# Performance work log

Measured on AMD Instinct MI355X. Metric: run time of the kernel, lower is better.

## Reference

```python
import jax, jax.numpy as jnp
import numpy as np

N_NODES = 512      # nodes in the original graph
N_SUB = 512        # NodeDeleted -> one subgraph per node
E_SUB = 2097152    # edges in the union-of-subgraphs graph (avg degree 8)
E_ORIG = 8192      # edges in the original graph
IN_DIM = 64
EMB = 64
L = 4
TASKS = 10


def setup_inputs() -> dict:
    key = jax.random.key(0)
    ks = jax.random.split(key, 16)
    NT = N_NODES * N_SUB
    x = jax.random.normal(ks[0], (NT, IN_DIM), jnp.float32)
    # edges stay within a subgraph: global id = subgraph_id * N + local id
    eg = jax.random.randint(ks[1], (E_SUB,), 0, N_SUB)
    src = jax.random.randint(ks[2], (E_SUB,), 0, N_NODES)
    dst = jax.random.randint(ks[3], (E_SUB,), 0, N_NODES)
    edge_index = jnp.stack([eg * N_NODES + src, eg * N_NODES + dst]).astype(jnp.int32)
    original_edge_index = jax.random.randint(ks[4], (2, E_ORIG), 0, N_NODES).astype(jnp.int32)
    subgraph_node_idx = jnp.tile(jnp.arange(N_NODES, dtype=jnp.int32), N_SUB)
    subgraph_batch = jnp.repeat(jnp.arange(N_SUB, dtype=jnp.int32), N_NODES)
    p = lambda k, shape: jax.random.normal(k, shape, jnp.float32) * 0.05
    return dict(
        x=x,
        Wrel=p(ks[5], (L, EMB, IN_DIM)), brel=jnp.zeros((L, EMB), jnp.float32),
        Wroot=p(ks[6], (L, EMB, IN_DIM)),
        bn_gamma=jnp.ones((L, EMB), jnp.float32), bn_beta=jnp.zeros((L, EMB), jnp.float32),
        Wrel_s=p(ks[7], (L, EMB, IN_DIM)), brel_s=jnp.zeros((L, EMB), jnp.float32),
        Wroot_s=p(ks[8], (L, EMB, IN_DIM)),
        bns_gamma=jnp.ones((L, EMB), jnp.float32), bns_beta=jnp.zeros((L, EMB), jnp.float32),
        W1=p(ks[9], (2 * EMB, EMB)), b1=jnp.zeros((2 * EMB,), jnp.float32),
        W2=p(ks[10], (TASKS, 2 * EMB)), b2=jnp.zeros((TASKS,), jnp.float32),
        edge_index=edge_index, original_edge_index=original_edge_index,
        subgraph_node_idx=subgraph_node_idx, subgraph_batch=subgraph_batch,
        num_nodes_int=N_NODES,
    )


def _gconv(h, ei, Wr, br, Wt, n):
    # PyG GraphConv, aggr='add': lin_rel(sum_{j->i} x_j) + lin_root(x_i)
    agg = jax.ops.segment_sum(h[ei[0]], ei[1], num_segments=n)
    return agg @ Wr.T + br + h @ Wt.T


def _bn(h, g, b):
    # BatchNorm1d, training mode: biased batch stats, eps=1e-5
    mu = h.mean(0)
    var = ((h - mu) ** 2).mean(0)
    return (h - mu) * jax.lax.rsqrt(var + 1e-5) * g + b


def _smean(src, idx, n):
    s = jax.ops.segment_sum(src, idx, num_segments=n)
    c = jax.ops.segment_sum(jnp.ones((src.shape[0], 1), src.dtype), idx, num_segments=n)
    return s / jnp.maximum(c, 1.0)


def reference(x, Wrel, brel, Wroot, bn_gamma, bn_beta, Wrel_s, brel_s, Wroot_s,
              bns_gamma, bns_beta, W1, b1, W2, b2,
              edge_index, original_edge_index, subgraph_node_idx, subgraph_batch,
              num_nodes_int):
    N = num_nodes_int
    NT = x.shape[0]
    S = NT // N  # num_subgraphs
    h = x
    for i in range(Wrel.shape[0]):
        h1 = _bn(_gconv(h, edge_index, Wrel[i], brel[i], Wroot[i], NT),
                 bn_gamma[i], bn_beta[i])
        x_sum = _smean(h, subgraph_node_idx, N)              # [N, emb]
        h2 = _bn(_gconv(x_sum, original_edge_index, Wrel_s[i], brel_s[i], Wroot_s[i], N),
                 bns_gamma[i], bns_beta[i])
        h = jax.nn.relu(h1 + jnp.tile(h2, (S, 1)))           # broadcast h2 to every subgraph
    x_nodes = _smean(h, subgraph_node_idx, N)                # [N, emb]
    z = jax.nn.log_softmax(x_nodes, axis=-1)                 # log_softmax BEFORE final MLP (as in source)
    out = jax.nn.relu(z @ W1.T + b1) @ W2.T + b2             # [N, num_tasks]
    return out
```

## Files before the change

### kernel.cpp

```cpp
#include <hip/hip_runtime.h>
#include <math.h>

#define NT 262144
#define NS 512
#define ES 2097152
#define EO 8192
#define NLAYER 4
#define WROW 68
#define BSL 704
#define EREG 8192

typedef short bf16x8 __attribute__((ext_vector_type(8)));
typedef float f32x4 __attribute__((ext_vector_type(4)));

__device__ __forceinline__ void cvt_hilo(const float* v, bf16x8* hi, bf16x8* lo) {
    union U { bf16x8 v; unsigned u[4]; };
    U H, L;
    #pragma unroll
    for (int q = 0; q < 4; q++) {
        float v0 = v[2 * q], v1 = v[2 * q + 1];
        unsigned h01;
        asm("v_cvt_pk_bf16_f32 %0, %1, %2" : "=v"(h01) : "v"(v0), "v"(v1));
        float l0 = v0 - __uint_as_float(h01 << 16);
        float l1 = v1 - __uint_as_float(h01 & 0xffff0000u);
        unsigned l01;
        asm("v_cvt_pk_bf16_f32 %0, %1, %2" : "=v"(l01) : "v"(l0), "v"(l1));
        H.u[q] = h01; L.u[q] = l01;
    }
    *hi = H.v; *lo = L.v;
}

__global__ __launch_bounds__(256) void bucket_kernel(const int* __restrict__ ei,
        int* __restrict__ gcur, unsigned* __restrict__ rbuf) {
    __shared__ int lcnt[512];
    __shared__ int lcur[512];
    int p = blockIdx.x;
    int g = p & 7;
    int base = p * 4096;
    int tid = threadIdx.x;
    for (int t = tid; t < 512; t += 256) lcnt[t] = 0;
    __syncthreads();
    int subs[16];
    unsigned recs[16];
    #pragma unroll
    for (int j = 0; j < 16; j++) {
        int e = base + j * 256 + tid;
        int d = ei[ES + e];
        int srcl = ei[e] & 511;
        subs[j] = d >> 9;
        recs[j] = (unsigned)srcl | ((unsigned)(d & 511) << 16);
        atomicAdd(&lcnt[subs[j]], 1);
    }
    __syncthreads();
    for (int t = tid; t < 512; t += 256) {
        int c = lcnt[t];
        lcur[t] = c ? atomicAdd(&gcur[g * 512 + t], c) : 0;
    }
    __syncthreads();
    #pragma unroll
    for (int j = 0; j < 16; j++) {
        int s = subs[j];
        int pos = atomicAdd(&lcur[s], 1);
        if (pos < BSL) rbuf[((size_t)s * 8 + g) * BSL + pos] = recs[j];
    }
}

__global__ __launch_bounds__(512) void csr_sub_kernel(const int* __restrict__ gcur,
        const unsigned* __restrict__ rbuf, int* __restrict__ rowptr,
        unsigned short* __restrict__ ebuf) {
    __shared__ int sdeg[512];
    __shared__ int sscan[512];
    __shared__ int scur[512];
    __shared__ unsigned short erow[EREG];
    __shared__ int scnt[8];
    int s = blockIdx.x;
    int t = threadIdx.x;
    sdeg[t] = 0;
    if (t < 8) scnt[t] = min(gcur[t * 512 + s], BSL);
    unsigned* e32 = (unsigned*)erow;
    #pragma unroll
    for (int j = 0; j < 8; j++) e32[j * 512 + t] = 0x02000200u;
    __syncthreads();
    for (int g = 0; g < 8; g++) {
        int cg = scnt[g];
        const unsigned* rb = rbuf + ((size_t)s * 8 + g) * BSL;
        for (int i = t; i < cg; i += 512) atomicAdd(&sdeg[rb[i] >> 16], 1);
    }
    __syncthreads();
    int pdeg = (sdeg[t] + 3) & ~3;
    sscan[t] = pdeg;
    __syncthreads();
    for (int off = 1; off < 512; off <<= 1) {
        int x = (t >= off) ? sscan[t - off] : 0;
        __syncthreads();
        sscan[t] += x;
        __syncthreads();
    }
    int excl = sscan[t] - pdeg;
    scur[t] = excl;
    rowptr[s * 513 + t] = s * EREG + excl;
    if (t == 511) rowptr[s * 513 + 512] = s * EREG + sscan[511];
    __syncthreads();
    for (int g = 0; g < 8; g++) {
        int cg = scnt[g];
        const unsigned* rb = rbuf + ((size_t)s * 8 + g) * BSL;
        for (int i = t; i < cg; i += 512) {
            unsigned rec = rb[i];
            int pos = atomicAdd(&scur[rec >> 16], 1);
            erow[pos] = (unsigned short)(rec & 511);
        }
    }
    __syncthreads();
    uint4* eo = (uint4*)(ebuf + (size_t)s * EREG);
    const uint4* ei4 = (const uint4*)erow;
    eo[t] = ei4[t];
    eo[t + 512] = ei4[t + 512];
}

__global__ void small_csr_kernel(const int* __restrict__ oei, int* __restrict__ rowptrS,
                                 int* __restrict__ srcsS) {
    __shared__ int sdeg[NS];
    __shared__ int scur[NS];
    int t = threadIdx.x;
    if (t < NS) sdeg[t] = 0;
    __syncthreads();
    for (int e = t; e < EO; e += 1024) atomicAdd(&sdeg[oei[EO + e]], 1);
    __syncthreads();
    int myv = (t < NS) ? sdeg[t] : 0;
    __syncthreads();
    for (int off = 1; off < NS; off <<= 1) {
        int x = (t >= off && t < NS) ? sdeg[t - off] : 0;
        __syncthreads();
        if (t < NS) sdeg[t] += x;
        __syncthreads();
    }
    if (t < NS) {
        int excl = sdeg[t] - myv;
        rowptrS[t] = excl;
        scur[t] = excl;
        if (t == 0) rowptrS[NS] = EO;
    }
    __syncthreads();
    for (int e = t; e < EO; e += 1024) {
        int d = oei[EO + e];
        int pos = atomicAdd(&scur[d], 1);
        srcsS[pos] = oei[e];
    }
}

__global__ __launch_bounds__(512, 2) void gconv_sub_kernel(
    const float* __restrict__ hsrc,
    const float* __restrict__ h2,
    const float* __restrict__ stB, const float* __restrict__ stS,
    const float* __restrict__ gB, const float* __restrict__ bB,
    const float* __restrict__ gS, const float* __restrict__ bS,
    int mode,
    const int* __restrict__ rowptr, const unsigned short* __restrict__ ebuf,
    const float* __restrict__ Wr, const float* __restrict__ Wt,
    const float* __restrict__ br,
    float* __restrict__ hout, float* __restrict__ stats)
{
    extern __shared__ char smem[];
    float* Wn = (float*)smem;
    float* bnp = Wn + 513 * WROW;

    int p = blockIdx.x;
    int sub = p;
    int tid = threadIdx.x;
    int w = tid >> 6;
    int l = tid & 63;
    int cl = l & 15;
    int kg = l >> 4;
    int kg8 = kg * 8;
    int half = w >> 2;
    int m = w & 3;

    if (mode) {
        if (tid < 64) {
            int c = tid;
            float sb = 0.f, qb = 0.f, ss = 0.f, qs = 0.f;
            for (int r2 = 0; r2 < 32; r2++) {
                sb += stB[r2 * 128 + c];
                qb += stB[r2 * 128 + 64 + c];
                ss += stS[r2 * 128 + c];
                qs += stS[r2 * 128 + 64 + c];
            }
            float muB = sb * (1.f / 262144.f);
            float varB = qb * (1.f / 262144.f) - muB * muB;
            float scB = gB[c] * rsqrtf(varB + 1e-5f);
            bnp[c] = scB;
            bnp[64 + c] = bB[c] - muB * scB;
            float muS = ss * (1.f / 512.f);
            float varS = qs * (1.f / 512.f) - muS * muS;
            float scS = gS[c] * rsqrtf(varS + 1e-5f);
            bnp[128 + c] = scS;
            bnp[192 + c] = bS[c] - muS * scS;
        }
        __syncthreads();
    }

    const float* srcbase = hsrc + (size_t)sub * 512 * 64;
    for (int idx = tid; idx < 512 * 16; idx += 512) {
        int r = idx >> 4;
        int c4 = (idx & 15) * 4;
        float4 a = *(const float4*)(srcbase + r * 64 + c4);
        if (mode) {
            float4 b = *(const float4*)(h2 + r * 64 + c4);
            float4 sB4 = *(const float4*)(bnp + c4);
            float4 hB4 = *(const float4*)(bnp + 64 + c4);
            float4 sS4 = *(const float4*)(bnp + 128 + c4);
            float4 hS4 = *(const float4*)(bnp + 192 + c4);
            a.x = fmaxf(a.x * sB4.x + hB4.x + b.x * sS4.x + hS4.x, 0.f);
            a.y = fmaxf(a.y * sB4.y + hB4.y + b.y * sS4.y + hS4.y, 0.f);
            a.z = fmaxf(a.z * sB4.z + hB4.z + b.z * sS4.z + hS4.z, 0.f);
            a.w = fmaxf(a.w * sB4.w + hB4.w + b.w * sS4.w + hS4.w, 0.f);
        }
        *(float4*)(Wn + r * WROW + c4) = a;
    }
    if (tid < WROW) Wn[512 * WROW + tid] = 0.f;

    bf16x8 Bh[16], Bl[16];
    float bias0, bias1, bias2, bias3;
    #pragma unroll
    for (int c = 0; c < 4; c++) {
        int col = c * 16 + cl;
        #pragma unroll
        for (int ch = 0; ch < 4; ch++) {
            const float* mat = (ch < 2) ? Wr : Wt;
            int k = (ch & 1) * 32 + kg8;
            float vv[8];
            *(float4*)vv = *(const float4*)(mat + col * 64 + k);
            *(float4*)(vv + 4) = *(const float4*)(mat + col * 64 + k + 4);
            cvt_hilo(vv, &Bh[c * 4 + ch], &Bl[c * 4 + ch]);
        }
    }
    bias0 = br[cl];
    bias1 = br[16 + cl];
    bias2 = br[32 + cl];
    bias3 = br[48 + cl];

    const uint2* ebuf2 = (const uint2*)ebuf;
    __syncthreads();

#define GATH1(qv) { \
        const float* pp = Wn + (qv) * WROW + kg8; \
        float4 tg0 = *(const float4*)(pp); \
        float4 tg1 = *(const float4*)(pp + 4); \
        float4 tg2 = *(const float4*)(pp + 32); \
        float4 tg3 = *(const float4*)(pp + 36); \
        a0.x += tg0.x; a0.y += tg0.y; a0.z += tg0.z; a0.w += tg0.w; \
        a1.x += tg1.x; a1.y += tg1.y; a1.z += tg1.z; a1.w += tg1.w; \
        a2.x += tg2.x; a2.y += tg2.y; a2.z += tg2.z; a2.w += tg2.w; \
        a3.x += tg3.x; a3.y += tg3.y; a3.z += tg3.z; a3.w += tg3.w; \
    }

#define DO_CHUNK(g0h, g1h, ch) { \
        float gg[8]; \
        *(float4*)gg = g0h; *(float4*)(gg + 4) = g1h; \
        bf16x8 ah, al; \
        cvt_hilo(gg, &ah, &al); \
        acc0 = __builtin_amdgcn_mfma_f32_16x16x32_bf16(ah, Bh[0 * 4 + ch], acc0, 0, 0, 0); \
        acc1 = __builtin_amdgcn_mfma_f32_16x16x32_bf16(ah, Bh[1 * 4 + ch], acc1, 0, 0, 0); \
        acc2 = __builtin_amdgcn_mfma_f32_16x16x32_bf16(ah, Bh[2 * 4 + ch], acc2, 0, 0, 0); \
        acc3 = __builtin_amdgcn_mfma_f32_16x16x32_bf16(ah, Bh[3 * 4 + ch], acc3, 0, 0, 0); \
        acc0 = __builtin_amdgcn_mfma_f32_16x16x32_bf16(al, Bh[0 * 4 + ch], acc0, 0, 0, 0); \
        acc1 = __builtin_amdgcn_mfma_f32_16x16x32_bf16(al, Bh[1 * 4 + ch], acc1, 0, 0, 0); \
        acc2 = __builtin_amdgcn_mfma_f32_16x16x32_bf16(al, Bh[2 * 4 + ch], acc2, 0, 0, 0); \
        acc3 = __builtin_amdgcn_mfma_f32_16x16x32_bf16(al, Bh[3 * 4 + ch], acc3, 0, 0, 0); \
        acc0 = __builtin_amdgcn_mfma_f32_16x16x32_bf16(ah, Bl[0 * 4 + ch], acc0, 0, 0, 0); \
        acc1 = __builtin_amdgcn_mfma_f32_16x16x32_bf16(ah, Bl[1 * 4 + ch], acc1, 0, 0, 0); \
        acc2 = __builtin_amdgcn_mfma_f32_16x16x32_bf16(ah, Bl[2 * 4 + ch], acc2, 0, 0, 0); \
        acc3 = __builtin_amdgcn_mfma_f32_16x16x32_bf16(ah, Bl[3 * 4 + ch], acc3, 0, 0, 0); \
    }

    float s0 = 0.f, s1 = 0.f, s2 = 0.f, s3 = 0.f;
    float q0s = 0.f, q1s = 0.f, q2s = 0.f, q3s = 0.f;

    for (int tt = 0; tt < 4; tt++) {
        int tile = half * 4 + tt;
        int nb = sub * 512 + tile * 64;
        int row = tile * 64 + m * 16 + cl;
        int rpb = sub * 513;
        int e0q = rowptr[rpb + row] >> 2;
        int e1q = rowptr[rpb + row + 1] >> 2;

        float4 a0 = make_float4(0.f, 0.f, 0.f, 0.f);
        float4 a1 = a0, a2 = a0, a3 = a0;
        uint2 rr = make_uint2(0u, 0u);
        int u = e0q;
        if (u < e1q) rr = ebuf2[u];
        while (u < e1q) {
            uint2 cur = rr;
            ++u;
            if (u < e1q) rr = ebuf2[u];
            unsigned q0 = cur.x & 0xffffu;
            unsigned q1 = cur.x >> 16;
            unsigned q2 = cur.y & 0xffffu;
            unsigned q3 = cur.y >> 16;
            GATH1(q0);
            GATH1(q1);
            GATH1(q2);
            GATH1(q3);
        }

        const float* wrow = Wn + (size_t)(tile * 64 + m * 16 + cl) * WROW + kg8;
        float4 r0 = *(const float4*)(wrow);
        float4 r1 = *(const float4*)(wrow + 4);
        float4 r2 = *(const float4*)(wrow + 32);
        float4 r3 = *(const float4*)(wrow + 36);

        f32x4 acc0, acc1, acc2, acc3;
        #pragma unroll
        for (int j = 0; j < 4; j++) {
            acc0[j] = bias0; acc1[j] = bias1; acc2[j] = bias2; acc3[j] = bias3;
        }
        DO_CHUNK(a0, a1, 0);
        DO_CHUNK(a2, a3, 1);
        DO_CHUNK(r0, r1, 2);
        DO_CHUNK(r2, r3, 3);

        int node0 = nb + m * 16 + kg * 4;
        #pragma unroll
        for (int j = 0; j < 4; j++) {
            float v0 = acc0[j], v1 = acc1[j], v2 = acc2[j], v3 = acc3[j];
            size_t rowb = (size_t)(node0 + j) * 64;
            hout[rowb + cl] = v0;
            hout[rowb + 16 + cl] = v1;
            hout[rowb + 32 + cl] = v2;
            hout[rowb + 48 + cl] = v3;
            s0 += v0; q0s += v0 * v0;
            s1 += v1; q1s += v1 * v1;
            s2 += v2; q2s += v2 * v2;
            s3 += v3; q3s += v3 * v3;
        }
    }

    s0 += __shfl_xor(s0, 16, 64); s0 += __shfl_xor(s0, 32, 64);
    s1 += __shfl_xor(s1, 16, 64); s1 += __shfl_xor(s1, 32, 64);
    s2 += __shfl_xor(s2, 16, 64); s2 += __shfl_xor(s2, 32, 64);
    s3 += __shfl_xor(s3, 16, 64); s3 += __shfl_xor(s3, 32, 64);
    q0s += __shfl_xor(q0s, 16, 64); q0s += __shfl_xor(q0s, 32, 64);
    q1s += __shfl_xor(q1s, 16, 64); q1s += __shfl_xor(q1s, 32, 64);
    q2s += __shfl_xor(q2s, 16, 64); q2s += __shfl_xor(q2s, 32, 64);
    q3s += __shfl_xor(q3s, 16, 64); q3s += __shfl_xor(q3s, 32, 64);
    if (kg == 0) {
        int rep = p & 31;
        atomicAdd(&stats[rep * 128 + cl], s0);
        atomicAdd(&stats[rep * 128 + 16 + cl], s1);
        atomicAdd(&stats[rep * 128 + 32 + cl], s2);
        atomicAdd(&stats[rep * 128 + 48 + cl], s3);
        atomicAdd(&stats[rep * 128 + 64 + cl], q0s);
        atomicAdd(&stats[rep * 128 + 80 + cl], q1s);
        atomicAdd(&stats[rep * 128 + 96 + cl], q2s);
        atomicAdd(&stats[rep * 128 + 112 + cl], q3s);
    }
#undef GATH1
#undef DO_CHUNK
}

__global__ __launch_bounds__(512, 6) void gconv_kernel(
    const float* __restrict__ hin, const int* __restrict__ rowptr, const int* __restrict__ srcs,
    const float* __restrict__ Wr, const float* __restrict__ Wt, const float* __restrict__ br,
    float* __restrict__ hout, float* __restrict__ stats)
{
    __shared__ float wrt[4096];
    __shared__ float wtt[4096];
    __shared__ float4 aggT[8][64];
    __shared__ float4 hT[8][64];
    __shared__ float sbuf[8][64];
    __shared__ float qbuf[8][64];
    __shared__ float brs[64];

    int tid = threadIdx.x;
    for (int idx = tid; idx < 4096; idx += 512) {
        int cc = idx >> 6, kk = idx & 63;
        wrt[kk * 64 + ((kk + cc) & 63)] = Wr[idx];
        wtt[kk * 64 + ((kk + cc) & 63)] = Wt[idx];
    }
    if (tid < 64) brs[tid] = br[tid];
    __syncthreads();

    int w = tid >> 6;
    int c = tid & 63;
    int node0 = (blockIdx.x * 8 + w) * 4;

    float* aggp = (float*)&aggT[w][0];
    float* hp   = (float*)&hT[w][0];
    #pragma unroll
    for (int r = 0; r < 4; r++) {
        int node = node0 + r;
        hp[c * 4 + r] = hin[node * 64 + c];
        int e0 = rowptr[node], e1 = rowptr[node + 1];
        float a = 0.f;
        int e = e0;
        for (; e + 4 <= e1; e += 4) {
            int s0 = srcs[e], s1 = srcs[e + 1], s2 = srcs[e + 2], s3 = srcs[e + 3];
            float v0 = hin[s0 * 64 + c];
            float v1 = hin[s1 * 64 + c];
            float v2 = hin[s2 * 64 + c];
            float v3 = hin[s3 * 64 + c];
            a += (v0 + v1) + (v2 + v3);
        }
        for (; e < e1; e++) a += hin[srcs[e] * 64 + c];
        aggp[c * 4 + r] = a;
    }

    float o0 = brs[c], o1 = o0, o2 = o0, o3 = o0;
    #pragma unroll 8
    for (int k = 0; k < 64; k++) {
        float wr = wrt[k * 64 + ((k + c) & 63)];
        float wt = wtt[k * 64 + ((k + c) & 63)];
        float4 av = aggT[w][k];
        float4 hv = hT[w][k];
        o0 += wr * av.x + wt * hv.x;
        o1 += wr * av.y + wt * hv.y;
        o2 += wr * av.z + wt * hv.z;
        o3 += wr * av.w + wt * hv.w;
    }
    hout[(node0 + 0) * 64 + c] = o0;
    hout[(node0 + 1) * 64 + c] = o1;
    hout[(node0 + 2) * 64 + c] = o2;
    hout[(node0 + 3) * 64 + c] = o3;

    sbuf[w][c] = (o0 + o1) + (o2 + o3);
    qbuf[w][c] = (o0 * o0 + o1 * o1) + (o2 * o2 + o3 * o3);
    __syncthreads();
    int rep = blockIdx.x & 31;
    if (w == 0) {
        float s = 0.f;
        #pragma unroll
        for (int ww = 0; ww < 8; ww++) s += sbuf[ww][c];
        atomicAdd(&stats[rep * 128 + c], s);
    } else if (w == 1) {
        float q = 0.f;
        #pragma unroll
        for (int ww = 0; ww < 8; ww++) q += qbuf[ww][c];
        atomicAdd(&stats[rep * 128 + 64 + c], q);
    }
}

__global__ __launch_bounds__(1024) void xsum_kernel(
    const float* __restrict__ hsrc, const float* __restrict__ h2,
    const float* __restrict__ stB, const float* __restrict__ stS,
    const float* __restrict__ gB, const float* __restrict__ bB,
    const float* __restrict__ gS, const float* __restrict__ bS,
    int mode, float* __restrict__ xsum)
{
    __shared__ float bnp[256];
    __shared__ float red[16][64];
    int t = threadIdx.x;
    if (mode) {
        if (t < 64) {
            int c = t;
            float sb = 0.f, qb = 0.f, ss = 0.f, qs = 0.f;
            for (int r2 = 0; r2 < 32; r2++) {
                sb += stB[r2 * 128 + c];
                qb += stB[r2 * 128 + 64 + c];
                ss += stS[r2 * 128 + c];
                qs += stS[r2 * 128 + 64 + c];
            }
            float muB = sb * (1.f / 262144.f);
            float varB = qb * (1.f / 262144.f) - muB * muB;
            float scB = gB[c] * rsqrtf(varB + 1e-5f);
            bnp[c] = scB;
            bnp[64 + c] = bB[c] - muB * scB;
            float muS = ss * (1.f / 512.f);
            float varS = qs * (1.f / 512.f) - muS * muS;
            float scS = gS[c] * rsqrtf(varS + 1e-5f);
            bnp[128 + c] = scS;
            bnp[192 + c] = bS[c] - muS * scS;
        }
        __syncthreads();
    }

    int w = t >> 6;
    int l = t & 63;
    int c4 = (l & 15) * 4;
    int r = l >> 4;
    int n = blockIdx.x;

    float bx = 0.f, by = 0.f, bz = 0.f, bw = 0.f;
    float4 sB = make_float4(1.f, 1.f, 1.f, 1.f);
    float4 hB = make_float4(0.f, 0.f, 0.f, 0.f);
    if (mode) {
        sB = *(const float4*)(bnp + c4);
        hB = *(const float4*)(bnp + 64 + c4);
        float4 sS = *(const float4*)(bnp + 128 + c4);
        float4 hS = *(const float4*)(bnp + 192 + c4);
        float4 b2 = *(const float4*)(h2 + n * 64 + c4);
        bx = b2.x * sS.x + hS.x;
        by = b2.y * sS.y + hS.y;
        bz = b2.z * sS.z + hS.z;
        bw = b2.w * sS.w + hS.w;
    }

    float4 acc = make_float4(0.f, 0.f, 0.f, 0.f);
    #pragma unroll
    for (int j = 0; j < 8; j++) {
        int si = w * 32 + j * 4 + r;
        size_t base = (size_t)(si * 512 + n) * 64 + c4;
        float4 a = *(const float4*)(hsrc + base);
        float4 v;
        if (mode) {
            v.x = fmaxf(a.x * sB.x + hB.x + bx, 0.f);
            v.y = fmaxf(a.y * sB.y + hB.y + by, 0.f);
            v.z = fmaxf(a.z * sB.z + hB.z + bz, 0.f);
            v.w = fmaxf(a.w * sB.w + hB.w + bw, 0.f);
        } else {
            v = a;
        }
        acc.x += v.x; acc.y += v.y; acc.z += v.z; acc.w += v.w;
    }
    acc.x += __shfl_xor(acc.x, 16, 64); acc.y += __shfl_xor(acc.y, 16, 64);
    acc.z += __shfl_xor(acc.z, 16, 64); acc.w += __shfl_xor(acc.w, 16, 64);
    acc.x += __shfl_xor(acc.x, 32, 64); acc.y += __shfl_xor(acc.y, 32, 64);
    acc.z += __shfl_xor(acc.z, 32, 64); acc.w += __shfl_xor(acc.w, 32, 64);
    if (l < 16) {
        red[w][c4 + 0] = acc.x;
        red[w][c4 + 1] = acc.y;
        red[w][c4 + 2] = acc.z;
        red[w][c4 + 3] = acc.w;
    }
    __syncthreads();
    if (t < 64) {
        float tot = 0.f;
        #pragma unroll
        for (int ww = 0; ww < 16; ww++) tot += red[ww][t];
        xsum[n * 64 + t] = tot * (1.f / 512.f);
    }
}

__global__ void head_kernel(const float* __restrict__ xs, const float* __restrict__ W1,
                            const float* __restrict__ b1, const float* __restrict__ W2,
                            const float* __restrict__ b2, float* __restrict__ out) {
    __shared__ float z[64];
    __shared__ float hid[128];
    int t = threadIdx.x;
    int n = blockIdx.x;
    if (t < 64) {
        float v = xs[n * 64 + t];
        float m = v;
        for (int off = 32; off >= 1; off >>= 1) m = fmaxf(m, __shfl_xor(m, off, 64));
        float e = expf(v - m);
        float s = e;
        for (int off = 32; off >= 1; off >>= 1) s += __shfl_xor(s, off, 64);
        z[t] = v - m - logf(s);
    }
    __syncthreads();
    {
        float acc = b1[t];
        const float* wrow = W1 + t * 64;
        #pragma unroll 8
        for (int k = 0; k < 64; k++) acc += z[k] * wrow[k];
        hid[t] = fmaxf(acc, 0.f);
    }
    __syncthreads();
    if (t < 10) {
        float o = b2[t];
        const float* wrow = W2 + t * 128;
        #pragma unroll 8
        for (int j = 0; j < 128; j++) o += hid[j] * wrow[j];
        out[n * 10 + t] = o;
    }
}

extern "C" void kernel_launch(void* const* d_in, const int* in_sizes, int n_in,
                              void* d_out, int out_size, void* d_ws, size_t ws_size,
                              hipStream_t stream) {
    const float* x       = (const float*)d_in[0];
    const float* Wrel    = (const float*)d_in[1];
    const float* brel    = (const float*)d_in[2];
    const float* Wroot   = (const float*)d_in[3];
    const float* bn_g    = (const float*)d_in[4];
    const float* bn_b    = (const float*)d_in[5];
    const float* Wrel_s  = (const float*)d_in[6];
    const float* brel_s  = (const float*)d_in[7];
    const float* Wroot_s = (const float*)d_in[8];
    const float* bns_g   = (const float*)d_in[9];
    const float* bns_b   = (const float*)d_in[10];
    const float* W1      = (const float*)d_in[11];
    const float* b1      = (const float*)d_in[12];
    const float* W2      = (const float*)d_in[13];
    const float* b2      = (const float*)d_in[14];
    const int* ei        = (const int*)d_in[15];
    const int* oei       = (const int*)d_in[16];
    float* out = (float*)d_out;

    char* ws = (char*)d_ws;
    size_t off = 0;
    auto alloc = [&](size_t bytes) -> void* {
        void* p = ws + off;
        off = (off + bytes + 255) & ~(size_t)255;
        return p;
    };
    float* h1    = (float*)alloc((size_t)NT * 64 * 4);
    float* xsum  = (float*)alloc(NS * 64 * 4);
    float* h2    = (float*)alloc(NS * 64 * 4);
    float* stats = (float*)alloc(NLAYER * 2 * 4096 * 4);
    int* rowptr  = (int*)alloc((size_t)NS * 513 * 4);
    int* gcur    = (int*)alloc(8 * 512 * 4);
    unsigned short* ebuf = (unsigned short*)alloc((size_t)NS * EREG * 2);
    int* rowptrS = (int*)alloc(513 * 4);
    int* srcsS   = (int*)alloc(EO * 4);
    unsigned* rbuf = (unsigned*)h1;
    (void)ws_size; (void)in_sizes; (void)n_in; (void)out_size;

    hipMemsetAsync(gcur, 0, 8 * 512 * 4, stream);
    hipMemsetAsync(stats, 0, (size_t)NLAYER * 2 * 4096 * 4, stream);

    bucket_kernel<<<ES / 4096, 256, 0, stream>>>(ei, gcur, rbuf);
    csr_sub_kernel<<<NS, 512, 0, stream>>>(gcur, rbuf, rowptr, ebuf);
    small_csr_kernel<<<1, 1024, 0, stream>>>(oei, rowptrS, srcsS);

    const size_t SMEM = (513 * WROW + 256) * 4;

    for (int i = 0; i < NLAYER; i++) {
        int mode = (i > 0);
        const float* hsrc = mode ? h1 : x;
        const float* stPB = stats + (i - 1) * 8192;
        const float* stPS = stPB + 4096;
        const float* gBp = bn_g + (i - 1) * 64;
        const float* bBp = bn_b + (i - 1) * 64;
        const float* gSp = bns_g + (i - 1) * 64;
        const float* bSp = bns_b + (i - 1) * 64;
        float* stB = stats + i * 8192;
        float* stS = stB + 4096;

        xsum_kernel<<<NS, 1024, 0, stream>>>(hsrc, h2, stPB, stPS, gBp, bBp, gSp, bSp,
                                             mode, xsum);
        gconv_sub_kernel<<<NS, 512, SMEM, stream>>>(hsrc, h2, stPB, stPS,
            gBp, bBp, gSp, bSp, mode, rowptr, ebuf,
            Wrel + i * 4096, Wroot + i * 4096, brel + i * 64, h1, stB);
        gconv_kernel<<<NS / 32, 512, 0, stream>>>(xsum, rowptrS, srcsS,
            Wrel_s + i * 4096, Wroot_s + i * 4096, brel_s + i * 64, h2, stS);
    }
    {
        const float* stPB = stats + 3 * 8192;
        const float* stPS = stPB + 4096;
        xsum_kernel<<<NS, 1024, 0, stream>>>(h1, h2, stPB, stPS,
            bn_g + 3 * 64, bn_b + 3 * 64, bns_g + 3 * 64, bns_b + 3 * 64, 1, xsum);
    }
    head_kernel<<<NS, 128, 0, stream>>>(xsum, W1, b1, W2, b2, out);
}
```

Baseline: 568.7 us.

## Fuse small-graph GraphConv into subgraph kernel and store node features as fp16 in LDS

New measurement: 716.5 us. +26.0%, slower.

```diff
diff --git a/kernel.cpp b/kernel.cpp
--- a/kernel.cpp
+++ b/kernel.cpp
@@ -6,12 +6,14 @@
 #define ES 2097152
 #define EO 8192
 #define NLAYER 4
-#define WROW 68
+#define WROWH 72
 #define BSL 704
 #define EREG 8192
 
 typedef short bf16x8 __attribute__((ext_vector_type(8)));
 typedef float f32x4 __attribute__((ext_vector_type(4)));
+typedef _Float16 half8 __attribute__((ext_vector_type(8)));
+typedef _Float16 half4v __attribute__((ext_vector_type(4)));
 
 __device__ __forceinline__ void cvt_hilo(const float* v, bf16x8* hi, bf16x8* lo) {
     union U { bf16x8 v; unsigned u[4]; };
@@ -148,7 +150,7 @@
     }
 }
 
-__global__ __launch_bounds__(512, 2) void gconv_sub_kernel(
+__global__ __launch_bounds__(512, 4) void gconv_sub_kernel(
     const float* __restrict__ hsrc,
     const float* __restrict__ h2,
     const float* __restrict__ stB, const float* __restrict__ stS,
@@ -158,15 +160,98 @@
     const int* __restrict__ rowptr, const unsigned short* __restrict__ ebuf,
     const float* __restrict__ Wr, const float* __restrict__ Wt,
     const float* __restrict__ br,
-    float* __restrict__ hout, float* __restrict__ stats)
+    float* __restrict__ hout, float* __restrict__ stats,
+    const float* __restrict__ xsumIn, const int* __restrict__ rowptrS,
+    const int* __restrict__ srcsS, const float* __restrict__ WrS,
+    const float* __restrict__ WtS, const float* __restrict__ brS,
+    float* __restrict__ h2out, float* __restrict__ statsS)
 {
     extern __shared__ char smem[];
-    float* Wn = (float*)smem;
-    float* bnp = Wn + 513 * WROW;
+    int tid = threadIdx.x;
+
+    if (blockIdx.x >= NS) {
+        float* wrt = (float*)smem;
+        float* wtt = wrt + 4096;
+        float4* aggT = (float4*)(wtt + 4096);
+        float4* hT = aggT + 8 * 64;
+        float* sbuf = (float*)(hT + 8 * 64);
+        float* qbuf = sbuf + 512;
+        float* brs = qbuf + 512;
+        int b2 = blockIdx.x - NS;
+
+        for (int idx = tid; idx < 4096; idx += 512) {
+            int cc = idx >> 6, kk = idx & 63;
+            wrt[kk * 64 + ((kk + cc) & 63)] = WrS[idx];
+            wtt[kk * 64 + ((kk + cc) & 63)] = WtS[idx];
+        }
+        if (tid < 64) brs[tid] = brS[tid];
+        __syncthreads();
+
+        int w = tid >> 6;
+        int c = tid & 63;
+        int node0 = (b2 * 8 + w) * 4;
+
+        float* aggp = (float*)&aggT[w * 64];
+        float* hp   = (float*)&hT[w * 64];
+        #pragma unroll
+        for (int r = 0; r < 4; r++) {
+            int node = node0 + r;
+            hp[c * 4 + r] = xsumIn[node * 64 + c];
+            int e0 = rowptrS[node], e1 = rowptrS[node + 1];
+            float a = 0.f;
+            int e = e0;
+            for (; e + 4 <= e1; e += 4) {
+                int s0 = srcsS[e], s1 = srcsS[e + 1], s2 = srcsS[e + 2], s3 = srcsS[e + 3];
+                float v0 = xsumIn[s0 * 64 + c];
+                float v1 = xsumIn[s1 * 64 + c];
+                float v2 = xsumIn[s2 * 64 + c];
+                float v3 = xsumIn[s3 * 64 + c];
+                a += (v0 + v1) + (v2 + v3);
+            }
+            for (; e < e1; e++) a += xsumIn[srcsS[e] * 64 + c];
+            aggp[c * 4 + r] = a;
+        }
+
+        float o0 = brs[c], o1 = o0, o2 = o0, o3 = o0;
+        #pragma unroll 8
+        for (int k = 0; k < 64; k++) {
+            float wr = wrt[k * 64 + ((k + c) & 63)];
+            float wt = wtt[k * 64 + ((k + c) & 63)];
+            float4 av = aggT[w * 64 + k];
+            float4 hv = hT[w * 64 + k];
+            o0 += wr * av.x + wt * hv.x;
+            o1 += wr * av.y + wt * hv.y;
+            o2 += wr * av.z + wt * hv.z;
+            o3 += wr * av.w + wt * hv.w;
+        }
+        h2out[(node0 + 0) * 64 + c] = o0;
+        h2out[(node0 + 1) * 64 + c] = o1;
+        h2out[(node0 + 2) * 64 + c] = o2;
+        h2out[(node0 + 3) * 64 + c] = o3;
+
+        sbuf[w * 64 + c] = (o0 + o1) + (o2 + o3);
+        qbuf[w * 64 + c] = (o0 * o0 + o1 * o1) + (o2 * o2 + o3 * o3);
+        __syncthreads();
+        int rep = b2 & 31;
+        if (w == 0) {
+            float s = 0.f;
+            #pragma unroll
+            for (int ww = 0; ww < 8; ww++) s += sbuf[ww * 64 + c];
+            atomicAdd(&statsS[rep * 128 + c], s);
+        } else if (w == 1) {
+            float q = 0.f;
+            #pragma unroll
+            for (int ww = 0; ww < 8; ww++) q += qbuf[ww * 64 + c];
+            atomicAdd(&statsS[rep * 128 + 64 + c], q);
+        }
+        return;
+    }
+
+    _Float16* WnH = (_Float16*)smem;
+    float* bnp = (float*)(smem + 513 * WROWH * 2);
 
     int p = blockIdx.x;
     int sub = p;
-    int tid = threadIdx.x;
     int w = tid >> 6;
     int l = tid & 63;
     int cl = l & 15;
@@ -215,9 +300,12 @@
             a.z = fmaxf(a.z * sB4.z + hB4.z + b.z * sS4.z + hS4.z, 0.f);
             a.w = fmaxf(a.w * sB4.w + hB4.w + b.w * sS4.w + hS4.w, 0.f);
         }
-        *(float4*)(Wn + r * WROW + c4) = a;
-    }
-    if (tid < WROW) Wn[512 * WROW + tid] = 0.f;
+        half4v hv;
+        hv[0] = (_Float16)a.x; hv[1] = (_Float16)a.y;
+        hv[2] = (_Float16)a.z; hv[3] = (_Float16)a.w;
+        *(half4v*)(WnH + r * WROWH + c4) = hv;
+    }
+    if (tid < 32) ((unsigned*)(WnH + 512 * WROWH))[tid] = 0u;
 
     bf16x8 Bh[16], Bl[16];
     float bias0, bias1, bias2, bias3;
@@ -243,15 +331,13 @@
     __syncthreads();
 
 #define GATH1(qv) { \
-        const float* pp = Wn + (qv) * WROW + kg8; \
-        float4 tg0 = *(const float4*)(pp); \
-        float4 tg1 = *(const float4*)(pp + 4); \
-        float4 tg2 = *(const float4*)(pp + 32); \
-        float4 tg3 = *(const float4*)(pp + 36); \
-        a0.x += tg0.x; a0.y += tg0.y; a0.z += tg0.z; a0.w += tg0.w; \
-        a1.x += tg1.x; a1.y += tg1.y; a1.z += tg1.z; a1.w += tg1.w; \
-        a2.x += tg2.x; a2.y += tg2.y; a2.z += tg2.z; a2.w += tg2.w; \
-        a3.x += tg3.x; a3.y += tg3.y; a3.z += tg3.z; a3.w += tg3.w; \
+        const _Float16* pp = WnH + (unsigned)(qv) * WROWH + kg8; \
+        half8 h0 = *(const half8*)(pp); \
+        half8 h1v = *(const half8*)(pp + 32); \
+        a0.x += (float)h0[0]; a0.y += (float)h0[1]; a0.z += (float)h0[2]; a0.w += (float)h0[3]; \
+        a1.x += (float)h0[4]; a1.y += (float)h0[5]; a1.z += (float)h0[6]; a1.w += (float)h0[7]; \
+        a2.x += (float)h1v[0]; a2.y += (float)h1v[1]; a2.z += (float)h1v[2]; a2.w += (float)h1v[3]; \
+        a3.x += (float)h1v[4]; a3.y += (float)h1v[5]; a3.z += (float)h1v[6]; a3.w += (float)h1v[7]; \
     }
 
 #define DO_CHUNK(g0h, g1h, ch) { \
@@ -303,11 +389,13 @@
             GATH1(q3);
         }
 
-        const float* wrow = Wn + (size_t)(tile * 64 + m * 16 + cl) * WROW + kg8;
-        float4 r0 = *(const float4*)(wrow);
-        float4 r1 = *(const float4*)(wrow + 4);
-        float4 r2 = *(const float4*)(wrow + 32);
-        float4 r3 = *(const float4*)(wrow + 36);
+        const _Float16* wrowH = WnH + (unsigned)(tile * 64 + m * 16 + cl) * WROWH + kg8;
+        half8 rh0 = *(const half8*)(wrowH);
+        half8 rh1 = *(const half8*)(wrowH + 32);
+        float4 r0 = make_float4((float)rh0[0], (float)rh0[1], (float)rh0[2], (float)rh0[3]);
+        float4 r1 = make_float4((float)rh0[4], (float)rh0[5], (float)rh0[6], (float)rh0[7]);
+        float4 r2 = make_float4((float)rh1[0], (float)rh1[1], (float)rh1[2], (float)rh1[3]);
+        float4 r3 = make_float4((float)rh1[4], (float)rh1[5], (float)rh1[6], (float)rh1[7]);
 
         f32x4 acc0, acc1, acc2, acc3;
         #pragma unroll
@@ -356,87 +444,6 @@
     }
 #undef GATH1
 #undef DO_CHUNK
-}
-
-__global__ __launch_bounds__(512, 6) void gconv_kernel(
-    const float* __restrict__ hin, const int* __restrict__ rowptr, const int* __restrict__ srcs,
-    const float* __restrict__ Wr, const float* __restrict__ Wt, const float* __restrict__ br,
-    float* __restrict__ hout, float* __restrict__ stats)
-{
-    __shared__ float wrt[4096];
-    __shared__ float wtt[4096];
-    __shared__ float4 aggT[8][64];
-    __shared__ float4 hT[8][64];
-    __shared__ float sbuf[8][64];
-    __shared__ float qbuf[8][64];
-    __shared__ float brs[64];
-
-    int tid = threadIdx.x;
-    for (int idx = tid; idx < 4096; idx += 512) {
-        int cc = idx >> 6, kk = idx & 63;
-        wrt[kk * 64 + ((kk + cc) & 63)] = Wr[idx];
-        wtt[kk * 64 + ((kk + cc) & 63)] = Wt[idx];
-    }
-    if (tid < 64) brs[tid] = br[tid];
-    __syncthreads();
-
-    int w = tid >> 6;
-    int c = tid & 63;
-    int node0 = (blockIdx.x * 8 + w) * 4;
-
-    float* aggp = (float*)&aggT[w][0];
-    float* hp   = (float*)&hT[w][0];
-    #pragma unroll
-    for (int r = 0; r < 4; r++) {
-        int node = node0 + r;
-        hp[c * 4 + r] = hin[node * 64 + c];
-        int e0 = rowptr[node], e1 = rowptr[node + 1];
-        float a = 0.f;
-        int e = e0;
-        for (; e + 4 <= e1; e += 4) {
-            int s0 = srcs[e], s1 = srcs[e + 1], s2 = srcs[e + 2], s3 = srcs[e + 3];
-            float v0 = hin[s0 * 64 + c];
-            float v1 = hin[s1 * 64 + c];
-            float v2 = hin[s2 * 64 + c];
-            float v3 = hin[s3 * 64 + c];
-            a += (v0 + v1) + (v2 + v3);
-        }
-        for (; e < e1; e++) a += hin[srcs[e] * 64 + c];
-        aggp[c * 4 + r] = a;
-    }
-
-    float o0 = brs[c], o1 = o0, o2 = o0, o3 = o0;
-    #pragma unroll 8
-    for (int k = 0; k < 64; k++) {
-        float wr = wrt[k * 64 + ((k + c) & 63)];
-        float wt = wtt[k * 64 + ((k + c) & 63)];
-        float4 av = aggT[w][k];
-        float4 hv = hT[w][k];
-        o0 += wr * av.x + wt * hv.x;
-        o1 += wr * av.y + wt * hv.y;
-        o2 += wr * av.z + wt * hv.z;
-        o3 += wr * av.w + wt * hv.w;
-    }
-    hout[(node0 + 0) * 64 + c] = o0;
-    hout[(node0 + 1) * 64 + c] = o1;
-    hout[(node0 + 2) * 64 + c] = o2;
-    hout[(node0 + 3) * 64 + c] = o3;
-
-    sbuf[w][c] = (o0 + o1) + (o2 + o3);
-    qbuf[w][c] = (o0 * o0 + o1 * o1) + (o2 * o2 + o3 * o3);
-    __syncthreads();
-    int rep = blockIdx.x & 31;
-    if (w == 0) {
-        float s = 0.f;
-        #pragma unroll
-        for (int ww = 0; ww < 8; ww++) s += sbuf[ww][c];
-        atomicAdd(&stats[rep * 128 + c], s);
-    } else if (w == 1) {
-        float q = 0.f;
-        #pragma unroll
-        for (int ww = 0; ww < 8; ww++) q += qbuf[ww][c];
-        atomicAdd(&stats[rep * 128 + 64 + c], q);
-    }
 }
 
 __global__ __launch_bounds__(1024) void xsum_kernel(
@@ -595,7 +602,7 @@
     };
     float* h1    = (float*)alloc((size_t)NT * 64 * 4);
     float* xsum  = (float*)alloc(NS * 64 * 4);
-    float* h2    = (float*)alloc(NS * 64 * 4);
+    float* h2buf = (float*)alloc((size_t)2 * NS * 64 * 4);
     float* stats = (float*)alloc(NLAYER * 2 * 4096 * 4);
     int* rowptr  = (int*)alloc((size_t)NS * 513 * 4);
     int* gcur    = (int*)alloc(8 * 512 * 4);
@@ -612,11 +619,13 @@
     csr_sub_kernel<<<NS, 512, 0, stream>>>(gcur, rbuf, rowptr, ebuf);
     small_csr_kernel<<<1, 1024, 0, stream>>>(oei, rowptrS, srcsS);
 
-    const size_t SMEM = (513 * WROW + 256) * 4;
+    const size_t SMEM = (size_t)513 * WROWH * 2 + 256 * 4;
 
     for (int i = 0; i < NLAYER; i++) {
         int mode = (i > 0);
         const float* hsrc = mode ? h1 : x;
+        const float* h2R = h2buf + (size_t)((i - 1) & 1) * NS * 64;
+        float* h2W = h2buf + (size_t)(i & 1) * NS * 64;
         const float* stPB = stats + (i - 1) * 8192;
         const float* stPS = stPB + 4096;
         const float* gBp = bn_g + (i - 1) * 64;
@@ -626,18 +635,19 @@
         float* stB = stats + i * 8192;
         float* stS = stB + 4096;
 
-        xsum_kernel<<<NS, 1024, 0, stream>>>(hsrc, h2, stPB, stPS, gBp, bBp, gSp, bSp,
+        xsum_kernel<<<NS, 1024, 0, stream>>>(hsrc, h2R, stPB, stPS, gBp, bBp, gSp, bSp,
                                              mode, xsum);
-        gconv_sub_kernel<<<NS, 512, SMEM, stream>>>(hsrc, h2, stPB, stPS,
+        gconv_sub_kernel<<<NS + 16, 512, SMEM, stream>>>(hsrc, h2R, stPB, stPS,
             gBp, bBp, gSp, bSp, mode, rowptr, ebuf,
-            Wrel + i * 4096, Wroot + i * 4096, brel + i * 64, h1, stB);
-        gconv_kernel<<<NS / 32, 512, 0, stream>>>(xsum, rowptrS, srcsS,
-            Wrel_s + i * 4096, Wroot_s + i * 4096, brel_s + i * 64, h2, stS);
+            Wrel + i * 4096, Wroot + i * 4096, brel + i * 64, h1, stB,
+            xsum, rowptrS, srcsS,
+            Wrel_s + i * 4096, Wroot_s + i * 4096, brel_s + i * 64, h2W, stS);
     }
     {
         const float* stPB = stats + 3 * 8192;
         const float* stPS = stPB + 4096;
-        xsum_kernel<<<NS, 1024, 0, stream>>>(h1, h2, stPB, stPS,
+        const float* h2R = h2buf + (size_t)(3 & 1) * NS * 64;
+        xsum_kernel<<<NS, 1024, 0, stream>>>(h1, h2R, stPB, stPS,
             bn_g + 3 * 64, bn_b + 3 * 64, bns_g + 3 * 64, bns_b + 3 * 64, 1, xsum);
     }
     head_kernel<<<NS, 128, 0, stream>>>(xsum, W1, b1, W2, b2, out);
```
